# Performance work log

Hardware: AMD Instinct MI355X
Metric: run time of the kernel (lower is better)

## Reference

```python
import jax, jax.numpy as jnp
import numpy as np

N_NODES = 50000
N_EDGES = 800000
IN_DIM = 50
HIDDEN = 256
N_CLASSES = 121
EPS = 1e-12


def setup_inputs() -> dict:
    key = jax.random.key(0)
    ks = jax.random.split(key, 12)
    p = lambda i, shape: (jax.random.normal(ks[i], shape, dtype=jnp.float32) * 0.05)
    x = jax.random.normal(ks[0], (N_NODES, IN_DIM), dtype=jnp.float32)
    edge_index = jax.random.randint(ks[1], (2, N_EDGES), 0, N_NODES, dtype=jnp.int64)
    return {
        "x": x,
        "edge_index": edge_index,
        # SAGEConv layer 1: lin_l (aggregated, with bias), lin_r (root, no bias)
        "w1_l": p(2, (IN_DIM, HIDDEN)), "b1": p(3, (HIDDEN,)), "w1_r": p(4, (IN_DIM, HIDDEN)),
        # parallel Linear 1
        "wl1": p(5, (IN_DIM, HIDDEN)), "bl1": p(6, (HIDDEN,)),
        # SAGEConv layer 2
        "w2_l": p(7, (HIDDEN, N_CLASSES)), "b2": p(8, (N_CLASSES,)), "w2_r": p(9, (HIDDEN, N_CLASSES)),
        # parallel Linear 2
        "wl2": p(10, (HIDDEN, N_CLASSES)), "bl2": p(11, (N_CLASSES,)),
    }


def _sage_conv(x, src, dst, w_l, b, w_r):
    # mean-aggregate source features at destination nodes (PyG SAGEConv, aggr='mean')
    n = x.shape[0]
    agg = jax.ops.segment_sum(x[src], dst, num_segments=n)            # [N, d]
    deg = jax.ops.segment_sum(jnp.ones((src.shape[0], 1), x.dtype), dst, num_segments=n)
    mean = agg / jnp.maximum(deg, 1.0)
    out = mean @ w_l + b + x @ w_r
    # normalize=True -> L2 row normalization (F.normalize semantics)
    norm = jnp.sqrt(jnp.sum(out * out, axis=-1, keepdims=True))
    return out / jnp.maximum(norm, EPS)


def reference(x, edge_index, w1_l, b1, w1_r, wl1, bl1, w2_l, b2, w2_r, wl2, bl2):
    src, dst = edge_index[0], edge_index[1]
    h = jax.nn.elu(_sage_conv(x, src, dst, w1_l, b1, w1_r) + (x @ wl1 + bl1))
    out = _sage_conv(h, src, dst, w2_l, b2, w2_r) + (h @ wl2 + bl2)
    return out
```

## Files before the change

kernel.cpp:

```cpp
#include <hip/hip_runtime.h>
#include <hip/hip_bf16.h>
#include <math.h>

typedef __hip_bfloat16 bf16;
typedef __attribute__((ext_vector_type(8))) short short8;
typedef __attribute__((ext_vector_type(4))) float f32x4;

#define N_NODES 50000
#define N_EDGES 800000
#define IN_DIM 50
#define HIDDEN 256
#define NCLS 121
#define PSTR 128
#define NCOLT 24
#define LDSPITCH 264
#define NCHUNK 196

#define OFF_OFF   50048
#define OFF_CSR   150160
#define OFF_HB    950272
#define OFF_PB    7350272
#define OFF_AB    10550272
#define OFF_XB    13750272
#define OFF_QRB   15000272
#define OFF_QLB   18200272
#define OFF_BW    21400272
#define OFF_BW1   21449424
#define OFF_CSUM  21482240
#define OFF_CBASE 21482496

__device__ __forceinline__ int clampi(int v, int hi) {
    return v < 0 ? 0 : (v >= hi ? hi - 1 : v);
}

__global__ __launch_bounds__(256) void prep_r18(
    const float* __restrict__ x, bf16* __restrict__ xb, bf16* __restrict__ ab,
    const float* __restrict__ w1l, const float* __restrict__ w1r,
    const float* __restrict__ wl1, bf16* __restrict__ bw1,
    const float* __restrict__ w2l, const float* __restrict__ w2r,
    const float* __restrict__ wl2, bf16* __restrict__ bw,
    int* __restrict__ degi) {
    int b = blockIdx.x;
    if (b < 25000) {
        int i = b * 256 + threadIdx.x;
        int n = i >> 7, c = i & 127;
        float v = 0.0f;
        if (c >= 64 && c < 64 + IN_DIM) v = x[n * IN_DIM + (c - 64)];
        ab[i] = __float2bfloat16(v);
        if (c < IN_DIM) xb[n * IN_DIM + c] = __float2bfloat16(x[n * IN_DIM + c]);
    } else if (b < 25256) {
        int i = (b - 25000) * 256 + threadIdx.x;
        int kt = i / 16384, r = i % 16384, c = r / 32, t32 = r % 32;
        int q = t32 >> 3, j = t32 & 7;
        int k = kt * 32 + q * 8 + j;
        float v = 0.0f;
        if (k < 64) {
            if (k < IN_DIM && c < 256) v = w1l[k * HIDDEN + c];
        } else {
            int kr = k - 64;
            if (kr < IN_DIM)
                v = (c < 256) ? w1r[kr * HIDDEN + c] : wl1[kr * HIDDEN + (c - 256)];
        }
        bw1[i] = __float2bfloat16(v);
    } else if (b < 25640) {
        int i = (b - 25256) * 256 + threadIdx.x;
        int kt = i / 12288, r = i % 12288, c = r / 32, t32 = r % 32;
        int q = t32 >> 3, j = t32 & 7;
        int k = kt * 32 + q * 8 + j;
        int mat = c >> 7, cls = c & 127;
        float v = 0.0f;
        if (cls < NCLS) {
            const float* w = (mat == 0) ? w2l : ((mat == 1) ? w2r : wl2);
            v = w[k * NCLS + cls];
        }
        bw[i] = __float2bfloat16(v);
    } else {
        int i = (b - 25640) * 256 + threadIdx.x;
        if (i < N_NODES) degi[i] = 0;
    }
}

__global__ __launch_bounds__(256) void degrank_r18(const int* __restrict__ dst,
                                                   int* __restrict__ degi,
                                                   int* __restrict__ rank) {
    int e = blockIdx.x * 256 + threadIdx.x;
    if (e < N_EDGES) {
        int d = clampi(dst[e], N_NODES);
        rank[e] = atomicAdd(&degi[d], 1);
    }
}

__global__ __launch_bounds__(256) void chunksum_r18(const int* __restrict__ degi,
                                                    int* __restrict__ csum) {
    __shared__ int red[256];
    int i = blockIdx.x * 256 + threadIdx.x;
    red[threadIdx.x] = (i < N_NODES) ? degi[i] : 0;
    __syncthreads();
    for (int s = 128; s > 0; s >>= 1) {
        if (threadIdx.x < s) red[threadIdx.x] += red[threadIdx.x + s];
        __syncthreads();
    }
    if (threadIdx.x == 0) csum[blockIdx.x] = red[0];
}

__global__ __launch_bounds__(256) void scanchunks_r18(const int* __restrict__ csum,
                                                      int* __restrict__ cbase,
                                                      int* __restrict__ off) {
    __shared__ int s[256];
    int t = threadIdx.x;
    int v = (t < NCHUNK) ? csum[t] : 0;
    s[t] = v;
    __syncthreads();
    for (int d = 1; d < 256; d <<= 1) {
        int u = (t >= d) ? s[t - d] : 0;
        __syncthreads();
        s[t] += u;
        __syncthreads();
    }
    if (t < NCHUNK) cbase[t] = s[t] - v;
    if (t == 255) off[N_NODES] = s[255];
}

__global__ __launch_bounds__(256) void scatteroff_r18(const int* __restrict__ degi,
                                                      const int* __restrict__ cbase,
                                                      int* __restrict__ off) {
    __shared__ int s[256];
    int i = blockIdx.x * 256 + threadIdx.x;
    int t = threadIdx.x;
    int v = (i < N_NODES) ? degi[i] : 0;
    s[t] = v;
    __syncthreads();
    for (int d = 1; d < 256; d <<= 1) {
        int u = (t >= d) ? s[t - d] : 0;
        __syncthreads();
        s[t] += u;
        __syncthreads();
    }
    int ex = s[t] - v + cbase[blockIdx.x];
    if (i < N_NODES) off[i] = ex;
}

__global__ __launch_bounds__(256) void csrfill2_r18(const int* __restrict__ src,
                                                    const int* __restrict__ dst,
                                                    const int* __restrict__ rank,
                                                    const int* __restrict__ off,
                                                    int* __restrict__ csr) {
    int e = blockIdx.x * 256 + threadIdx.x;
    if (e >= N_EDGES) return;
    int d = clampi(dst[e], N_NODES);
    csr[off[d] + rank[e]] = clampi(src[e], N_NODES);
}

__global__ __launch_bounds__(256) void gather1_r18(
    const unsigned int* __restrict__ xbu, const int* __restrict__ off,
    const int* __restrict__ csr, const int* __restrict__ degi,
    unsigned int* __restrict__ abu) {
    __shared__ float rdeg[8];
    int base = blockIdx.x * 8;
    int tid = threadIdx.x;
    if (tid < 8) rdeg[tid] = 1.0f / fmaxf((float)degi[base + tid], 1.0f);
    __syncthreads();
    int wave = tid >> 6, lane = tid & 63;
    int half = lane >> 5, l = lane & 31;
    int n = wave * 2 + half;
    int node = base + n;
    int e0 = off[node], e1 = off[node + 1];
    if (l < 25) {
        float ax0 = 0, ay0 = 0, ax1 = 0, ay1 = 0;
        float ax2 = 0, ay2 = 0, ax3 = 0, ay3 = 0;
        int e = e0;
        for (; e + 4 <= e1; e += 4) {
            unsigned u0 = xbu[(size_t)csr[e] * 25 + l];
            unsigned u1 = xbu[(size_t)csr[e + 1] * 25 + l];
            unsigned u2 = xbu[(size_t)csr[e + 2] * 25 + l];
            unsigned u3 = xbu[(size_t)csr[e + 3] * 25 + l];
            ax0 += __uint_as_float(u0 << 16);
            ay0 += __uint_as_float(u0 & 0xffff0000u);
            ax1 += __uint_as_float(u1 << 16);
            ay1 += __uint_as_float(u1 & 0xffff0000u);
            ax2 += __uint_as_float(u2 << 16);
            ay2 += __uint_as_float(u2 & 0xffff0000u);
            ax3 += __uint_as_float(u3 << 16);
            ay3 += __uint_as_float(u3 & 0xffff0000u);
        }
        for (; e < e1; ++e) {
            unsigned u0 = xbu[(size_t)csr[e] * 25 + l];
            ax0 += __uint_as_float(u0 << 16);
            ay0 += __uint_as_float(u0 & 0xffff0000u);
        }
        float mx = ((ax0 + ax1) + (ax2 + ax3)) * rdeg[n];
        float my = ((ay0 + ay1) + (ay2 + ay3)) * rdeg[n];
        bf16 bx = __float2bfloat16(mx), by = __float2bfloat16(my);
        unsigned pack = (unsigned)*(unsigned short*)&bx |
                        ((unsigned)*(unsigned short*)&by << 16);
        abu[(size_t)node * 64 + l] = pack;
    }
}

__global__ __launch_bounds__(256) void proj1_r18(
    const bf16* __restrict__ ab_, const bf16* __restrict__ bw1,
    const float* __restrict__ b1, const float* __restrict__ bl1,
    bf16* __restrict__ hb) {
    __shared__ float os[16][516];
    __shared__ float partial[16][17];
    __shared__ float rns[16];

    int base = blockIdx.x * 16;
    int tid = threadIdx.x;
    int wave = tid >> 6, lane = tid & 63;
    int rc = lane & 15, quad = lane >> 4;

    const short* ab = (const short*)ab_;
    short8 af[4];
#pragma unroll
    for (int kt = 0; kt < 4; ++kt)
        af[kt] = *(const short8*)&ab[(size_t)(base + rc) * 128 + kt * 32 + quad * 8];

    const short* bws = (const short*)bw1;
    for (int ti = 0; ti < 8; ++ti) {
        int t = wave * 8 + ti;
        f32x4 acc = {0.0f, 0.0f, 0.0f, 0.0f};
#pragma unroll
        for (int kt = 0; kt < 4; ++kt) {
            short8 bf = *(const short8*)
                &bws[(((size_t)kt * 512 + t * 16 + rc) * 4 + quad) * 8];
            acc = __builtin_amdgcn_mfma_f32_16x16x32_bf16(af[kt], bf, acc, 0, 0, 0);
        }
        int col = t * 16 + rc;
#pragma unroll
        for (int r = 0; r < 4; ++r) os[quad * 4 + r][col] = acc[r];
    }
    __syncthreads();
    {
        int n = tid & 15, jj = tid >> 4;
        float s = 0.0f;
#pragma unroll
        for (int c = 0; c < 16; ++c) {
            int cc = jj * 16 + c;
            float v = os[n][cc] + b1[cc];
            s += v * v;
        }
        partial[n][jj] = s;
    }
    __syncthreads();
    if (tid < 16) {
        float s = 0.0f;
#pragma unroll
        for (int jj = 0; jj < 16; ++jj) s += partial[tid][jj];
        rns[tid] = 1.0f / fmaxf(sqrtf(s), 1e-12f);
    }
    __syncthreads();
    for (int i = 0; i < 16; ++i) {
        int idx = i * 256 + tid;
        int n = idx >> 8, c = idx & 255;
        float z = (os[n][c] + b1[c]) * rns[n] + os[n][256 + c] + bl1[c];
        hb[(size_t)(base + n) * HIDDEN + c] =
            __float2bfloat16(z > 0.0f ? z : expm1f(z));
    }
}

__global__ __launch_bounds__(256) void proj2_r18(
    const bf16* __restrict__ hb, const bf16* __restrict__ bw,
    bf16* __restrict__ pb, bf16* __restrict__ qrb, bf16* __restrict__ qlb) {
    __shared__ __align__(16) short hs_s[16 * LDSPITCH];

    int base = blockIdx.x * 16;
    int tid = threadIdx.x;
    {
        int row = tid >> 4, ch = tid & 15;
        const uint4* s =
            (const uint4*)((const short*)hb + (size_t)(base + row) * HIDDEN + ch * 16);
        uint4 v0 = s[0];
        *(uint4*)&hs_s[row * LDSPITCH + ch * 16] = v0;
    }
    {
        int row = tid >> 4, ch = tid & 15;
        const uint4* s =
            (const uint4*)((const short*)hb + (size_t)(base + row) * HIDDEN + ch * 16 + 8);
        uint4 v1 = s[0];
        *(uint4*)&hs_s[row * LDSPITCH + ch * 16 + 8] = v1;
    }
    __syncthreads();

    int wave = tid >> 6, lane = tid & 63;
    int rc = lane & 15, quad = lane >> 4;

    short8 af[8];
#pragma unroll
    for (int kt = 0; kt < 8; ++kt)
        af[kt] = *(const short8*)&hs_s[rc * LDSPITCH + kt * 32 + quad * 8];

    const short* bws = (const short*)bw;
    for (int ti = 0; ti < NCOLT / 4; ++ti) {
        int t = wave * (NCOLT / 4) + ti;
        f32x4 acc = {0.0f, 0.0f, 0.0f, 0.0f};
#pragma unroll
        for (int kt = 0; kt < 8; ++kt) {
            short8 bf = *(const short8*)
                &bws[(((size_t)kt * 384 + t * 16 + rc) * 4 + quad) * 8];
            acc = __builtin_amdgcn_mfma_f32_16x16x32_bf16(af[kt], bf, acc, 0, 0, 0);
        }
        int col = t * 16 + rc;
        int mat = col >> 7, cls = col & 127;
#pragma unroll
        for (int r = 0; r < 4; ++r) {
            int node = base + quad * 4 + r;
            bf16 v = __float2bfloat16(acc[r]);
            if (mat == 0)
                pb[(size_t)node * PSTR + cls] = v;
            else if (mat == 1)
                qrb[(size_t)node * PSTR + cls] = v;
            else
                qlb[(size_t)node * PSTR + cls] = v;
        }
    }
}

__global__ __launch_bounds__(256) void final_r18(
    const unsigned int* __restrict__ pbu, const bf16* __restrict__ qrb,
    const bf16* __restrict__ qlb, const int* __restrict__ off,
    const int* __restrict__ csr, const int* __restrict__ degi,
    const float* __restrict__ b2, const float* __restrict__ bl2,
    float* __restrict__ out) {
    __shared__ float mp[8][128];
    __shared__ float red[8][128];
    __shared__ float rdeg[8];

    int base = blockIdx.x * 8;
    int tid = threadIdx.x;
    if (tid < 8) rdeg[tid] = 1.0f / fmaxf((float)degi[base + tid], 1.0f);
    int wv = tid >> 6, lane = tid & 63;
#pragma unroll
    for (int i = 0; i < 2; ++i) {
        int n = wv * 2 + i;
        int node = base + n;
        int e0 = off[node], e1 = off[node + 1];
        float ax0 = 0, ay0 = 0, ax1 = 0, ay1 = 0;
        float ax2 = 0, ay2 = 0, ax3 = 0, ay3 = 0;
        int e = e0;
        for (; e + 4 <= e1; e += 4) {
            unsigned u0 = pbu[(size_t)csr[e] * 64 + lane];
            unsigned u1 = pbu[(size_t)csr[e + 1] * 64 + lane];
            unsigned u2 = pbu[(size_t)csr[e + 2] * 64 + lane];
            unsigned u3 = pbu[(size_t)csr[e + 3] * 64 + lane];
            ax0 += __uint_as_float(u0 << 16);
            ay0 += __uint_as_float(u0 & 0xffff0000u);
            ax1 += __uint_as_float(u1 << 16);
            ay1 += __uint_as_float(u1 & 0xffff0000u);
            ax2 += __uint_as_float(u2 << 16);
            ay2 += __uint_as_float(u2 & 0xffff0000u);
            ax3 += __uint_as_float(u3 << 16);
            ay3 += __uint_as_float(u3 & 0xffff0000u);
        }
        for (; e < e1; ++e) {
            unsigned u0 = pbu[(size_t)csr[e] * 64 + lane];
            ax0 += __uint_as_float(u0 << 16);
            ay0 += __uint_as_float(u0 & 0xffff0000u);
        }
        mp[n][2 * lane] = (ax0 + ax1) + (ax2 + ax3);
        mp[n][2 * lane + 1] = (ay0 + ay1) + (ay2 + ay3);
    }
    __syncthreads();

    int j = tid & 127, g = tid >> 7;
    float bj = (j < NCLS) ? b2[j] : 0.0f;
    float blj = (j < NCLS) ? bl2[j] : 0.0f;
    float out2[4];
#pragma unroll
    for (int i = 0; i < 4; ++i) {
        int n = g * 4 + i;
        out2[i] = (j < NCLS)
                      ? (mp[n][j] * rdeg[n] + bj +
                         __bfloat162float(qrb[(size_t)(base + n) * PSTR + j]))
                      : 0.0f;
        red[n][j] = out2[i] * out2[i];
    }
    __syncthreads();
    for (int stride = 64; stride > 0; stride >>= 1) {
        if (j < stride) {
#pragma unroll
            for (int i = 0; i < 4; ++i)
                red[g * 4 + i][j] += red[g * 4 + i][j + stride];
        }
        __syncthreads();
    }
    if (j < NCLS) {
#pragma unroll
        for (int i = 0; i < 4; ++i) {
            int n = g * 4 + i;
            float rn = 1.0f / fmaxf(sqrtf(red[n][0]), 1e-12f);
            out[(base + n) * NCLS + j] =
                out2[i] * rn +
                __bfloat162float(qlb[(size_t)(base + n) * PSTR + j]) + blj;
        }
    }
}

extern "C" void kernel_launch(void* const* d_in, const int* in_sizes, int n_in,
                              void* d_out, int out_size, void* d_ws, size_t ws_size,
                              hipStream_t stream) {
    const float* x   = (const float*)d_in[0];
    const int*   ei  = (const int*)d_in[1];
    const float* w1l = (const float*)d_in[2];
    const float* b1  = (const float*)d_in[3];
    const float* w1r = (const float*)d_in[4];
    const float* wl1 = (const float*)d_in[5];
    const float* bl1 = (const float*)d_in[6];
    const float* w2l = (const float*)d_in[7];
    const float* b2  = (const float*)d_in[8];
    const float* w2r = (const float*)d_in[9];
    const float* wl2 = (const float*)d_in[10];
    const float* bl2 = (const float*)d_in[11];
    float* out = (float*)d_out;

    const int* src = ei;
    const int* dst = ei + N_EDGES;

    int*   wsI   = (int*)d_ws;
    float* wsF   = (float*)d_ws;
    int*   degi  = wsI;
    int*   off   = wsI + OFF_OFF;
    int*   csr   = wsI + OFF_CSR;
    bf16*  hb    = (bf16*)(wsF + OFF_HB);
    int*   rank  = (int*)(wsF + OFF_HB);
    bf16*  pb    = (bf16*)(wsF + OFF_PB);
    bf16*  ab    = (bf16*)(wsF + OFF_AB);
    bf16*  xb    = (bf16*)(wsF + OFF_XB);
    bf16*  qrb   = (bf16*)(wsF + OFF_QRB);
    bf16*  qlb   = (bf16*)(wsF + OFF_QLB);
    bf16*  bw    = (bf16*)(wsF + OFF_BW);
    bf16*  bw1   = (bf16*)(wsF + OFF_BW1);
    int*   csum  = wsI + OFF_CSUM;
    int*   cbase = wsI + OFF_CBASE;

    prep_r18<<<25836, 256, 0, stream>>>(x, xb, ab, w1l, w1r, wl1, bw1,
                                        w2l, w2r, wl2, bw, degi);

    degrank_r18<<<(N_EDGES + 255) / 256, 256, 0, stream>>>(dst, degi, rank);

    chunksum_r18<<<NCHUNK, 256, 0, stream>>>(degi, csum);
    scanchunks_r18<<<1, 256, 0, stream>>>(csum, cbase, off);
    scatteroff_r18<<<NCHUNK, 256, 0, stream>>>(degi, cbase, off);

    csrfill2_r18<<<(N_EDGES + 255) / 256, 256, 0, stream>>>(src, dst, rank, off, csr);

    gather1_r18<<<N_NODES / 8, 256, 0, stream>>>((const unsigned int*)xb, off,
                                                 csr, degi, (unsigned int*)ab);
    proj1_r18<<<N_NODES / 16, 256, 0, stream>>>(ab, bw1, b1, bl1, hb);
    proj2_r18<<<N_NODES / 16, 256, 0, stream>>>(hb, bw, pb, qrb, qlb);
    final_r18<<<N_NODES / 8, 256, 0, stream>>>((const unsigned int*)pb, qrb, qlb,
                                               off, csr, degi, b2, bl2, out);
}
```

Measured before the change: 309.8 us.

## Widen proj2 row tile to 64 and vectorize final gather across half-waves

proj2 now processes 64 rows per block, in four 16-row groups, so each B-weight fragment loaded from global memory feeds four MFMAs instead of one. This cuts weight traffic and block count in exchange for more A-fragment registers and a partial last block, which is bounds-guarded on store. final's neighbor gather has each half-wave load 8-byte uint2 chunks of different edges, eight edges per iteration, and then combines the halves with a shuffle. This raises memory-level parallelism per lane. The rest is renaming plus a small bit-cast helper.

```diff
diff --git a/kernel.cpp b/kernel.cpp
--- a/kernel.cpp
+++ b/kernel.cpp
@@ -15,6 +15,7 @@
 #define NCOLT 24
 #define LDSPITCH 264
 #define NCHUNK 196
+#define P2ROWS 64
 
 #define OFF_OFF   50048
 #define OFF_CSR   150160
@@ -33,7 +34,9 @@
     return v < 0 ? 0 : (v >= hi ? hi - 1 : v);
 }
 
-__global__ __launch_bounds__(256) void prep_r18(
+__device__ __forceinline__ float uf(unsigned u) { return __uint_as_float(u); }
+
+__global__ __launch_bounds__(256) void prep_r19(
     const float* __restrict__ x, bf16* __restrict__ xb, bf16* __restrict__ ab,
     const float* __restrict__ w1l, const float* __restrict__ w1r,
     const float* __restrict__ wl1, bf16* __restrict__ bw1,
@@ -80,7 +83,7 @@
     }
 }
 
-__global__ __launch_bounds__(256) void degrank_r18(const int* __restrict__ dst,
+__global__ __launch_bounds__(256) void degrank_r19(const int* __restrict__ dst,
                                                    int* __restrict__ degi,
                                                    int* __restrict__ rank) {
     int e = blockIdx.x * 256 + threadIdx.x;
@@ -90,7 +93,7 @@
     }
 }
 
-__global__ __launch_bounds__(256) void chunksum_r18(const int* __restrict__ degi,
+__global__ __launch_bounds__(256) void chunksum_r19(const int* __restrict__ degi,
                                                     int* __restrict__ csum) {
     __shared__ int red[256];
     int i = blockIdx.x * 256 + threadIdx.x;
@@ -103,7 +106,7 @@
     if (threadIdx.x == 0) csum[blockIdx.x] = red[0];
 }
 
-__global__ __launch_bounds__(256) void scanchunks_r18(const int* __restrict__ csum,
+__global__ __launch_bounds__(256) void scanchunks_r19(const int* __restrict__ csum,
                                                       int* __restrict__ cbase,
                                                       int* __restrict__ off) {
     __shared__ int s[256];
@@ -121,7 +124,7 @@
     if (t == 255) off[N_NODES] = s[255];
 }
 
-__global__ __launch_bounds__(256) void scatteroff_r18(const int* __restrict__ degi,
+__global__ __launch_bounds__(256) void scatteroff_r19(const int* __restrict__ degi,
                                                       const int* __restrict__ cbase,
                                                       int* __restrict__ off) {
     __shared__ int s[256];
@@ -140,7 +143,7 @@
     if (i < N_NODES) off[i] = ex;
 }
 
-__global__ __launch_bounds__(256) void csrfill2_r18(const int* __restrict__ src,
+__global__ __launch_bounds__(256) void csrfill2_r19(const int* __restrict__ src,
                                                     const int* __restrict__ dst,
                                                     const int* __restrict__ rank,
                                                     const int* __restrict__ off,
@@ -151,7 +154,7 @@
     csr[off[d] + rank[e]] = clampi(src[e], N_NODES);
 }
 
-__global__ __launch_bounds__(256) void gather1_r18(
+__global__ __launch_bounds__(256) void gather1_r19(
     const unsigned int* __restrict__ xbu, const int* __restrict__ off,
     const int* __restrict__ csr, const int* __restrict__ degi,
     unsigned int* __restrict__ abu) {
@@ -174,19 +177,19 @@
             unsigned u1 = xbu[(size_t)csr[e + 1] * 25 + l];
             unsigned u2 = xbu[(size_t)csr[e + 2] * 25 + l];
             unsigned u3 = xbu[(size_t)csr[e + 3] * 25 + l];
-            ax0 += __uint_as_float(u0 << 16);
-            ay0 += __uint_as_float(u0 & 0xffff0000u);
-            ax1 += __uint_as_float(u1 << 16);
-            ay1 += __uint_as_float(u1 & 0xffff0000u);
-            ax2 += __uint_as_float(u2 << 16);
-            ay2 += __uint_as_float(u2 & 0xffff0000u);
-            ax3 += __uint_as_float(u3 << 16);
-            ay3 += __uint_as_float(u3 & 0xffff0000u);
+            ax0 += uf(u0 << 16);
+            ay0 += uf(u0 & 0xffff0000u);
+            ax1 += uf(u1 << 16);
+            ay1 += uf(u1 & 0xffff0000u);
+            ax2 += uf(u2 << 16);
+            ay2 += uf(u2 & 0xffff0000u);
+            ax3 += uf(u3 << 16);
+            ay3 += uf(u3 & 0xffff0000u);
         }
         for (; e < e1; ++e) {
             unsigned u0 = xbu[(size_t)csr[e] * 25 + l];
-            ax0 += __uint_as_float(u0 << 16);
-            ay0 += __uint_as_float(u0 & 0xffff0000u);
+            ax0 += uf(u0 << 16);
+            ay0 += uf(u0 & 0xffff0000u);
         }
         float mx = ((ax0 + ax1) + (ax2 + ax3)) * rdeg[n];
         float my = ((ay0 + ay1) + (ay2 + ay3)) * rdeg[n];
@@ -197,7 +200,7 @@
     }
 }
 
-__global__ __launch_bounds__(256) void proj1_r18(
+__global__ __launch_bounds__(256) void proj1_r19(
     const bf16* __restrict__ ab_, const bf16* __restrict__ bw1,
     const float* __restrict__ b1, const float* __restrict__ bl1,
     bf16* __restrict__ hb) {
@@ -259,65 +262,63 @@
     }
 }
 
-__global__ __launch_bounds__(256) void proj2_r18(
+__global__ __launch_bounds__(256) void proj2_r19(
     const bf16* __restrict__ hb, const bf16* __restrict__ bw,
     bf16* __restrict__ pb, bf16* __restrict__ qrb, bf16* __restrict__ qlb) {
-    __shared__ __align__(16) short hs_s[16 * LDSPITCH];
-
-    int base = blockIdx.x * 16;
+    __shared__ __align__(16) short hs[P2ROWS * LDSPITCH];
+
+    int base = blockIdx.x * P2ROWS;
     int tid = threadIdx.x;
-    {
-        int row = tid >> 4, ch = tid & 15;
-        const uint4* s =
-            (const uint4*)((const short*)hb + (size_t)(base + row) * HIDDEN + ch * 16);
-        uint4 v0 = s[0];
-        *(uint4*)&hs_s[row * LDSPITCH + ch * 16] = v0;
-    }
-    {
-        int row = tid >> 4, ch = tid & 15;
-        const uint4* s =
-            (const uint4*)((const short*)hb + (size_t)(base + row) * HIDDEN + ch * 16 + 8);
-        uint4 v1 = s[0];
-        *(uint4*)&hs_s[row * LDSPITCH + ch * 16 + 8] = v1;
+    const short* hbs = (const short*)hb;
+#pragma unroll
+    for (int i = 0; i < 8; ++i) {
+        int f = tid + 256 * i;
+        int row = f >> 5, u4 = f & 31;
+        *(uint4*)&hs[row * LDSPITCH + u4 * 8] =
+            *(const uint4*)(hbs + (size_t)(base + row) * HIDDEN + u4 * 8);
     }
     __syncthreads();
 
     int wave = tid >> 6, lane = tid & 63;
     int rc = lane & 15, quad = lane >> 4;
 
-    short8 af[8];
-#pragma unroll
-    for (int kt = 0; kt < 8; ++kt)
-        af[kt] = *(const short8*)&hs_s[rc * LDSPITCH + kt * 32 + quad * 8];
+    short8 af[4][8];
+#pragma unroll
+    for (int rg = 0; rg < 4; ++rg)
+#pragma unroll
+        for (int kt = 0; kt < 8; ++kt)
+            af[rg][kt] = *(const short8*)
+                &hs[(rg * 16 + rc) * LDSPITCH + kt * 32 + quad * 8];
 
     const short* bws = (const short*)bw;
-    for (int ti = 0; ti < NCOLT / 4; ++ti) {
-        int t = wave * (NCOLT / 4) + ti;
-        f32x4 acc = {0.0f, 0.0f, 0.0f, 0.0f};
+    for (int ti = 0; ti < 6; ++ti) {
+        int t = wave * 6 + ti;
+        f32x4 acc[4] = {{0, 0, 0, 0}, {0, 0, 0, 0}, {0, 0, 0, 0}, {0, 0, 0, 0}};
 #pragma unroll
         for (int kt = 0; kt < 8; ++kt) {
             short8 bf = *(const short8*)
                 &bws[(((size_t)kt * 384 + t * 16 + rc) * 4 + quad) * 8];
-            acc = __builtin_amdgcn_mfma_f32_16x16x32_bf16(af[kt], bf, acc, 0, 0, 0);
+#pragma unroll
+            for (int rg = 0; rg < 4; ++rg)
+                acc[rg] = __builtin_amdgcn_mfma_f32_16x16x32_bf16(af[rg][kt], bf,
+                                                                  acc[rg], 0, 0, 0);
         }
         int col = t * 16 + rc;
         int mat = col >> 7, cls = col & 127;
-#pragma unroll
-        for (int r = 0; r < 4; ++r) {
-            int node = base + quad * 4 + r;
-            bf16 v = __float2bfloat16(acc[r]);
-            if (mat == 0)
-                pb[(size_t)node * PSTR + cls] = v;
-            else if (mat == 1)
-                qrb[(size_t)node * PSTR + cls] = v;
-            else
-                qlb[(size_t)node * PSTR + cls] = v;
-        }
-    }
-}
-
-__global__ __launch_bounds__(256) void final_r18(
-    const unsigned int* __restrict__ pbu, const bf16* __restrict__ qrb,
+        bf16* dstp = (mat == 0) ? pb : ((mat == 1) ? qrb : qlb);
+#pragma unroll
+        for (int rg = 0; rg < 4; ++rg)
+#pragma unroll
+            for (int r = 0; r < 4; ++r) {
+                int node = base + rg * 16 + quad * 4 + r;
+                if (node < N_NODES)
+                    dstp[(size_t)node * PSTR + cls] = __float2bfloat16(acc[rg][r]);
+            }
+    }
+}
+
+__global__ __launch_bounds__(256) void final_r19(
+    const bf16* __restrict__ pb, const bf16* __restrict__ qrb,
     const bf16* __restrict__ qlb, const int* __restrict__ off,
     const int* __restrict__ csr, const int* __restrict__ degi,
     const float* __restrict__ b2, const float* __restrict__ bl2,
@@ -326,39 +327,72 @@
     __shared__ float red[8][128];
     __shared__ float rdeg[8];
 
+    const uint2* pbu2 = (const uint2*)pb;
     int base = blockIdx.x * 8;
     int tid = threadIdx.x;
     if (tid < 8) rdeg[tid] = 1.0f / fmaxf((float)degi[base + tid], 1.0f);
     int wv = tid >> 6, lane = tid & 63;
+    int h = lane >> 5, lh = lane & 31;
 #pragma unroll
     for (int i = 0; i < 2; ++i) {
         int n = wv * 2 + i;
         int node = base + n;
         int e0 = off[node], e1 = off[node + 1];
-        float ax0 = 0, ay0 = 0, ax1 = 0, ay1 = 0;
-        float ax2 = 0, ay2 = 0, ax3 = 0, ay3 = 0;
+        float c0 = 0, c1 = 0, c2 = 0, c3 = 0;
+        float d0 = 0, d1 = 0, d2 = 0, d3 = 0;
         int e = e0;
-        for (; e + 4 <= e1; e += 4) {
-            unsigned u0 = pbu[(size_t)csr[e] * 64 + lane];
-            unsigned u1 = pbu[(size_t)csr[e + 1] * 64 + lane];
-            unsigned u2 = pbu[(size_t)csr[e + 2] * 64 + lane];
-            unsigned u3 = pbu[(size_t)csr[e + 3] * 64 + lane];
-            ax0 += __uint_as_float(u0 << 16);
-            ay0 += __uint_as_float(u0 & 0xffff0000u);
-            ax1 += __uint_as_float(u1 << 16);
-            ay1 += __uint_as_float(u1 & 0xffff0000u);
-            ax2 += __uint_as_float(u2 << 16);
-            ay2 += __uint_as_float(u2 & 0xffff0000u);
-            ax3 += __uint_as_float(u3 << 16);
-            ay3 += __uint_as_float(u3 & 0xffff0000u);
-        }
-        for (; e < e1; ++e) {
-            unsigned u0 = pbu[(size_t)csr[e] * 64 + lane];
-            ax0 += __uint_as_float(u0 << 16);
-            ay0 += __uint_as_float(u0 & 0xffff0000u);
-        }
-        mp[n][2 * lane] = (ax0 + ax1) + (ax2 + ax3);
-        mp[n][2 * lane + 1] = (ay0 + ay1) + (ay2 + ay3);
+        for (; e + 8 <= e1; e += 8) {
+            int r0 = csr[e + h];
+            int r1 = csr[e + 2 + h];
+            int r2 = csr[e + 4 + h];
+            int r3 = csr[e + 6 + h];
+            uint2 u0 = pbu2[(size_t)r0 * 32 + lh];
+            uint2 u1 = pbu2[(size_t)r1 * 32 + lh];
+            uint2 u2 = pbu2[(size_t)r2 * 32 + lh];
+            uint2 u3 = pbu2[(size_t)r3 * 32 + lh];
+            c0 += uf(u0.x << 16);
+            c1 += uf(u0.x & 0xffff0000u);
+            c2 += uf(u0.y << 16);
+            c3 += uf(u0.y & 0xffff0000u);
+            d0 += uf(u1.x << 16);
+            d1 += uf(u1.x & 0xffff0000u);
+            d2 += uf(u1.y << 16);
+            d3 += uf(u1.y & 0xffff0000u);
+            c0 += uf(u2.x << 16);
+            c1 += uf(u2.x & 0xffff0000u);
+            c2 += uf(u2.y << 16);
+            c3 += uf(u2.y & 0xffff0000u);
+            d0 += uf(u3.x << 16);
+            d1 += uf(u3.x & 0xffff0000u);
+            d2 += uf(u3.y << 16);
+            d3 += uf(u3.y & 0xffff0000u);
+        }
+        for (; e < e1; e += 2) {
+            int idx = e + h;
+            int safe = idx < e1 ? idx : e;
+            int r0 = csr[safe];
+            uint2 u = pbu2[(size_t)r0 * 32 + lh];
+            if (idx < e1) {
+                c0 += uf(u.x << 16);
+                c1 += uf(u.x & 0xffff0000u);
+                c2 += uf(u.y << 16);
+                c3 += uf(u.y & 0xffff0000u);
+            }
+        }
+        c0 += d0;
+        c1 += d1;
+        c2 += d2;
+        c3 += d3;
+        c0 += __shfl_xor(c0, 32, 64);
+        c1 += __shfl_xor(c1, 32, 64);
+        c2 += __shfl_xor(c2, 32, 64);
+        c3 += __shfl_xor(c3, 32, 64);
+        if (h == 0) {
+            mp[n][4 * lh + 0] = c0;
+            mp[n][4 * lh + 1] = c1;
+            mp[n][4 * lh + 2] = c2;
+            mp[n][4 * lh + 3] = c3;
+        }
     }
     __syncthreads();
 
@@ -433,21 +467,21 @@
     int*   csum  = wsI + OFF_CSUM;
     int*   cbase = wsI + OFF_CBASE;
 
-    prep_r18<<<25836, 256, 0, stream>>>(x, xb, ab, w1l, w1r, wl1, bw1,
+    prep_r19<<<25836, 256, 0, stream>>>(x, xb, ab, w1l, w1r, wl1, bw1,
                                         w2l, w2r, wl2, bw, degi);
 
-    degrank_r18<<<(N_EDGES + 255) / 256, 256, 0, stream>>>(dst, degi, rank);
-
-    chunksum_r18<<<NCHUNK, 256, 0, stream>>>(degi, csum);
-    scanchunks_r18<<<1, 256, 0, stream>>>(csum, cbase, off);
-    scatteroff_r18<<<NCHUNK, 256, 0, stream>>>(degi, cbase, off);
-
-    csrfill2_r18<<<(N_EDGES + 255) / 256, 256, 0, stream>>>(src, dst, rank, off, csr);
-
-    gather1_r18<<<N_NODES / 8, 256, 0, stream>>>((const unsigned int*)xb, off,
+    degrank_r19<<<(N_EDGES + 255) / 256, 256, 0, stream>>>(dst, degi, rank);
+
+    chunksum_r19<<<NCHUNK, 256, 0, stream>>>(degi, csum);
+    scanchunks_r19<<<1, 256, 0, stream>>>(csum, cbase, off);
+    scatteroff_r19<<<NCHUNK, 256, 0, stream>>>(degi, cbase, off);
+
+    csrfill2_r19<<<(N_EDGES + 255) / 256, 256, 0, stream>>>(src, dst, rank, off, csr);
+
+    gather1_r19<<<N_NODES / 8, 256, 0, stream>>>((const unsigned int*)xb, off,
                                                  csr, degi, (unsigned int*)ab);
-    proj1_r18<<<N_NODES / 16, 256, 0, stream>>>(ab, bw1, b1, bl1, hb);
-    proj2_r18<<<N_NODES / 16, 256, 0, stream>>>(hb, bw, pb, qrb, qlb);
-    final_r18<<<N_NODES / 8, 256, 0, stream>>>((const unsigned int*)pb, qrb, qlb,
+    proj1_r19<<<N_NODES / 16, 256, 0, stream>>>(ab, bw1, b1, bl1, hb);
+    proj2_r19<<<(N_NODES + P2ROWS - 1) / P2ROWS, 256, 0, stream>>>(hb, bw, pb, qrb, qlb);
+    final_r19<<<N_NODES / 8, 256, 0, stream>>>(pb, qrb, qlb,
                                                off, csr, degi, b2, bl2, out);
 }
```

New measurement: 293.8 us. 5.2% less time.
